# Kernel optimization log

Hardware: AMD Instinct MI355X
Metric: run time of the kernel (lower is better)

The kernel has to match this reference:

```python
import jax, jax.numpy as jnp
import numpy as np
import math


def _extend(chunk):
    # chunk: [b, C, w, 1, dh] -> stacked (prev, cur, next) chunks: [b, C, w, 1, dh, 3]
    prev = jnp.pad(chunk[:, :-1], ((0, 0), (1, 0), (0, 0), (0, 0), (0, 0)))
    nxt = jnp.pad(chunk[:, 1:], ((0, 0), (0, 1), (0, 0), (0, 0), (0, 0)))
    return jnp.stack((prev, chunk, nxt), axis=-1)


def local_xl_attention(q, kv, Wq, Wkv, Wc, w):
    b, L, dm = q.shape
    dh = Wkv.shape[1] // 2          # d_head (w_kv projects to 2*d_head)
    nh = dm // dh                   # n_head
    C = L // w                      # number of chunks

    qp = (q @ Wq).reshape(b, L, nh, dh) / math.sqrt(dh)   # [b,L,nh,dh]
    kvp = kv @ Wkv                                         # [b,L,2*dh]
    k = kvp[..., :dh][:, :, None, :]                       # [b,L,1,dh] single KV head
    v = kvp[..., dh:][:, :, None, :]

    # sliding_chunks_matmul_qk (faithful to original einsum, incl. sum over z)
    cq = qp.reshape(b, C, w, nh, dh)
    ck_e = _extend(k.reshape(b, C, w, 1, dh))              # [b,C,w,1,dh,3]
    attn = jnp.einsum('bcxhd,bzyode->bcxhey', cq, ck_e)    # [b,C,w,nh,3,w]
    attn = attn.reshape(b, L, nh, 3 * w)

    probs = jax.nn.softmax(attn, axis=-1)

    # sliding_chunks_matmul_pv (faithful, incl. sum over z)
    cp = probs.reshape(b, C, w, nh, 3, w)
    cv_e = _extend(v.reshape(b, C, w, 1, dh))              # [b,C,w,1,dh,3]
    ctx = jnp.einsum('bcwhpd,bzdoep->bcwhe', cp, cv_e)     # [b,C,w,nh,dh]
    out = ctx.reshape(b, L, dm) @ Wc
    return out


def setup_inputs() -> dict:
    key = jax.random.key(0)
    ks = jax.random.split(key, 5)
    B, L, DM, NH = 1, 4096, 1024, 16
    DH = DM // NH
    scale = 0.02
    return {
        'q': jax.random.normal(ks[0], (B, L, DM), dtype=jnp.float32),
        'kv': jax.random.normal(ks[1], (B, L, DM), dtype=jnp.float32),
        'Wq': jax.random.normal(ks[2], (DM, DM), dtype=jnp.float32) * scale,
        'Wkv': jax.random.normal(ks[3], (DM, 2 * DH), dtype=jnp.float32) * scale,
        'Wc': jax.random.normal(ks[4], (DM, DM), dtype=jnp.float32) * scale,
        'w': 512,
    }


def reference(q, kv, Wq, Wkv, Wc, w):
    return local_xl_attention(q, kv, Wq, Wkv, Wc, w)
```

## Files before the change

kernel.cpp:

```cpp
#include <hip/hip_runtime.h>
#include <hip/hip_bf16.h>
#include <cstdint>
#include <cstddef>

#define L_ 4096
#define DM_ 1024
#define NH_ 16
#define DH_ 64
#define W_ 512
#define C_ 8
#define W3_ 1536
#define NROWS_ 65536

typedef __attribute__((ext_vector_type(8))) short short8;
typedef __attribute__((ext_vector_type(4))) float f32x4;

__device__ __forceinline__ void async16(const void* g, void* l) {
    __builtin_amdgcn_global_load_lds(
        (const __attribute__((address_space(1))) unsigned int*)g,
        (__attribute__((address_space(3))) unsigned int*)l, 16, 0, 0);
}

#if __has_builtin(__builtin_amdgcn_exp2f)
#define FEXP2(x) __builtin_amdgcn_exp2f(x)
#else
#define FEXP2(x) exp2f(x)
#endif

__device__ __forceinline__ int nanhit(unsigned u) {
    return (((u & 0x7F80u) == 0x7F80u) | (((u >> 16) & 0x7F80u) == 0x7F80u));
}
__global__ __launch_bounds__(256) void detect_kernel(const uint4* __restrict__ q,
                                                     int* __restrict__ flag) {
    __shared__ int s;
    if (threadIdx.x == 0) s = 0;
    __syncthreads();
    int hit = 0;
#pragma unroll
    for (int r = 0; r < 8; ++r) {
        uint4 v = q[threadIdx.x + 256 * r];
        hit |= nanhit(v.x) | nanhit(v.y) | nanhit(v.z) | nanhit(v.w);
    }
    if (__any(hit)) { if ((threadIdx.x & 63) == 0) atomicOr(&s, 1); }
    __syncthreads();
    if (threadIdx.x == 0) flag[0] = s;
}

__device__ __forceinline__ float ldf(const void* X, size_t i, int f32) {
    return f32 ? ((const float*)X)[i] : __bfloat162float(((const __hip_bfloat16*)X)[i]);
}

__global__ __launch_bounds__(256) void megaprep(const void* __restrict__ q,
                                                const void* __restrict__ kv,
                                                const void* __restrict__ Wq,
                                                const void* __restrict__ Wkv,
                                                const void* __restrict__ Wc,
                                                __hip_bfloat16* __restrict__ qbuf,
                                                __hip_bfloat16* __restrict__ WqT,
                                                __hip_bfloat16* __restrict__ WkvT,
                                                __hip_bfloat16* __restrict__ WcT,
                                                __hip_bfloat16* __restrict__ kvred,
                                                const int* __restrict__ flag) {
    __shared__ float t[64][65];
    const int b = blockIdx.x;
    const int f32 = flag[0];
    const int tid = threadIdx.x;

    if (b < 4096) {
        int i = (b * 256 + tid) * 4;
        if (f32) {
            float4 v = *(const float4*)((const float*)q + i);
            __hip_bfloat162 tmp[2] = {__float22bfloat162_rn({v.x, v.y}),
                                      __float22bfloat162_rn({v.z, v.w})};
            *(short4*)((short*)qbuf + i) = *(const short4*)tmp;
        } else {
            *(short4*)((short*)qbuf + i) = *(const short4*)((const short*)q + i);
        }
    } else if (b < 4640) {
        const void* W;
        __hip_bfloat16* WT;
        int K = 1024, N, n0, k0;
        if (b < 4352) {
            int bx = b - 4096; W = Wq; WT = WqT; N = 1024;
            n0 = (bx & 15) * 64; k0 = (bx >> 4) * 64;
        } else if (b < 4608) {
            int bx = b - 4352; W = Wc; WT = WcT; N = 1024;
            n0 = (bx & 15) * 64; k0 = (bx >> 4) * 64;
        } else {
            int bx = b - 4608; W = Wkv; WT = WkvT; N = 128;
            n0 = (bx & 1) * 64; k0 = (bx >> 1) * 64;
        }
        const int tx = tid & 63;
        const int ty = tid >> 6;
#pragma unroll
        for (int r = 0; r < 16; ++r) {
            int k = ty + r * 4;
            t[k][tx] = ldf(W, (size_t)(k0 + k) * N + n0 + tx, f32);
        }
        __syncthreads();
#pragma unroll
        for (int r = 0; r < 16; ++r) {
            int n = ty + r * 4;
            WT[(size_t)(n0 + n) * K + k0 + tx] = __float2bfloat16(t[tx][n]);
        }
    } else {
        int y2 = b - 4640;
        int c = tid * 4;
        float a0 = 0.f, a1 = 0.f, a2 = 0.f, a3 = 0.f;
        if (y2 < 512) {
#pragma unroll
            for (int z = 0; z < C_; ++z) {
                size_t base = (size_t)(z * W_ + y2) * 1024 + c;
                a0 += ldf(kv, base + 0, f32);
                a1 += ldf(kv, base + 1, f32);
                a2 += ldf(kv, base + 2, f32);
                a3 += ldf(kv, base + 3, f32);
            }
        } else {
            int row = (y2 < 1024) ? (y2 - 512) : (3584 + y2 - 1024);
            size_t base = (size_t)row * 1024 + c;
            a0 = ldf(kv, base + 0, f32);
            a1 = ldf(kv, base + 1, f32);
            a2 = ldf(kv, base + 2, f32);
            a3 = ldf(kv, base + 3, f32);
        }
        __hip_bfloat162 tmp[2] = {__float22bfloat162_rn({a0, a1}),
                                  __float22bfloat162_rn({a2, a3})};
        *(short4*)((short*)kvred + (size_t)y2 * 1024 + c) = *(const short4*)tmp;
    }
}

struct GemmP {
    const __hip_bfloat16* A;
    const __hip_bfloat16* BT;
    void* C;
    int M, N, K;
    float alpha;
    int cMode;
    int ntiles;
    int swz;
    int nblocks;
};

__global__ __launch_bounds__(256) void gemm_bt_mfma(GemmP p0, GemmP p1,
                                                    const int* __restrict__ flag) {
    __shared__ __hip_bfloat16 Asl[2][128 * 32];
    __shared__ __hip_bfloat16 Bsl[2][64 * 32];

    GemmP p;
    int bid;
    if ((int)blockIdx.x < p0.nblocks) { p = p0; bid = blockIdx.x; }
    else { p = p1; bid = (int)blockIdx.x - p0.nblocks; }

    int mt, nt;
    if (!p.swz) { mt = bid / p.ntiles; nt = bid % p.ntiles; }
    else {
        int g = bid / (8 * p.ntiles);
        int rem = bid % (8 * p.ntiles);
        mt = g * 8 + (rem & 7);
        nt = rem >> 3;
    }
    const int m0 = mt * 128;
    const int n0 = nt * 64;
    const int K = p.K;
    const int N = p.N;

    const int tid = threadIdx.x;
    const int lane = tid & 63;
    const int wv = tid >> 6;
    const int wm = wv >> 1;
    const int wn = wv & 1;
    const int col = lane & 15;
    const int quad = lane >> 4;

    const int srow = lane >> 2;
    const int scol = (lane & 3) * 8;
    const __hip_bfloat16* Ag = p.A + (size_t)m0 * K;
    const __hip_bfloat16* Bg = p.BT + (size_t)n0 * K;

    f32x4 acc[4][2] = {};

    for (int k0 = 0; k0 < K; k0 += 64) {
#pragma unroll
        for (int h = 0; h < 2; ++h) {
            int arow = wv * 32 + h * 16 + srow;
#pragma unroll
            for (int kc = 0; kc < 2; ++kc)
                async16(Ag + (size_t)arow * K + k0 + kc * 32 + scol,
                        &Asl[kc][arow * 32 + scol]);
        }
        {
            int brow = wv * 16 + srow;
#pragma unroll
            for (int kc = 0; kc < 2; ++kc)
                async16(Bg + (size_t)brow * K + k0 + kc * 32 + scol,
                        &Bsl[kc][brow * 32 + scol]);
        }
        __syncthreads();

#pragma unroll
        for (int kc = 0; kc < 2; ++kc) {
            short8 af[4], bfr[2];
#pragma unroll
            for (int i = 0; i < 4; ++i)
                af[i] = *(const short8*)(&Asl[kc][(wm * 64 + i * 16 + col) * 32 + quad * 8]);
#pragma unroll
            for (int j = 0; j < 2; ++j)
                bfr[j] = *(const short8*)(&Bsl[kc][(wn * 32 + j * 16 + col) * 32 + quad * 8]);
#pragma unroll
            for (int am = 0; am < 4; ++am)
#pragma unroll
                for (int bn = 0; bn < 2; ++bn)
                    acc[am][bn] = __builtin_amdgcn_mfma_f32_16x16x32_bf16(af[am], bfr[bn], acc[am][bn], 0, 0, 0);
        }
        __syncthreads();
    }

    int cF = (p.cMode == 1) ? 1 : ((p.cMode == 2) ? 0 : flag[0]);
#pragma unroll
    for (int am = 0; am < 4; ++am)
#pragma unroll
        for (int bn = 0; bn < 2; ++bn)
#pragma unroll
            for (int r = 0; r < 4; ++r) {
                size_t ci = (size_t)(m0 + wm * 64 + am * 16 + quad * 4 + r) * N
                            + n0 + wn * 32 + bn * 16 + col;
                float v = acc[am][bn][r] * p.alpha;
                if (cF) ((float*)p.C)[ci] = v;
                else ((__hip_bfloat16*)p.C)[ci] = __float2bfloat16(v);
            }
}

__global__ __launch_bounds__(256) void sums_kernel(const float* __restrict__ kvp_red,
                                                   __hip_bfloat16* __restrict__ Kb,
                                                   __hip_bfloat16* __restrict__ Vt) {
    int t = blockIdx.x * 256 + threadIdx.x;
    int d = t & 63;
    int y = t >> 6;

    float kc = kvp_red[(size_t)y * 128 + d];
    float kf = kvp_red[(size_t)(512 + y) * 128 + d];
    float kl = kvp_red[(size_t)(1024 + y) * 128 + d];
    float vc = kvp_red[(size_t)y * 128 + 64 + d];
    float vf = kvp_red[(size_t)(512 + y) * 128 + 64 + d];
    float vl = kvp_red[(size_t)(1024 + y) * 128 + 64 + d];

    float kvals[3] = {kc - kl, kc, kc - kf};
    float vvals[3] = {vc - vl, vc, vc - vf};
#pragma unroll
    for (int e = 0; e < 3; ++e) {
        int key = e * W_ + y;
        Kb[(size_t)key * 64 + d] = __float2bfloat16(kvals[e]);
        int g = key >> 6;
        int i = key & 63;
        int p = ((i & 15) << 2) | (i >> 4);
        Vt[(size_t)d * W3_ + g * 64 + p] = __float2bfloat16(vvals[e]);
    }
}

#define PSTRIDE 72
__global__ __launch_bounds__(256, 2) void attn_kernel(const __hip_bfloat16* __restrict__ qb,
                                                      const __hip_bfloat16* __restrict__ Kb,
                                                      const __hip_bfloat16* __restrict__ Vt,
                                                      __hip_bfloat16* __restrict__ ctx) {
    __shared__ __align__(16) char smem[36864 + 1024];
    float* Ls = (float*)smem;
    float* lsum = (float*)(smem + 36864);

    const int tid = threadIdx.x;
    const int lane = tid & 63;
    const int wv = tid >> 6;
    const int m0 = blockIdx.x * 64;
    const int col = lane & 15;
    const int quad = lane >> 4;
    __hip_bfloat16* pw = (__hip_bfloat16*)smem + wv * (64 * PSTRIDE);

    short8 qf[4][2];
#pragma unroll
    for (int rg = 0; rg < 4; ++rg) {
        const __hip_bfloat16* qp = qb + (size_t)(m0 + rg * 16 + col) * 64 + quad * 8;
        qf[rg][0] = *(const short8*)(qp);
        qf[rg][1] = *(const short8*)(qp + 32);
    }

    f32x4 O[4][4] = {};
    float lrow[4][4] = {};

    for (int t = 0; t < 6; ++t) {
        const int kt = wv * 384 + t * 64;

        short8 kb0[4], kb1[4];
#pragma unroll
        for (int f = 0; f < 4; ++f) {
            const __hip_bfloat16* kp = Kb + (size_t)(kt + f * 16 + col) * 64 + quad * 8;
            kb0[f] = *(const short8*)(kp);
            kb1[f] = *(const short8*)(kp + 32);
        }

#pragma unroll
        for (int rg = 0; rg < 4; ++rg) {
            f32x4 S[4];
            __builtin_amdgcn_s_setprio(1);
#pragma unroll
            for (int f = 0; f < 4; ++f) {
                f32x4 s = {};
                s = __builtin_amdgcn_mfma_f32_16x16x32_bf16(qf[rg][0], kb0[f], s, 0, 0, 0);
                s = __builtin_amdgcn_mfma_f32_16x16x32_bf16(qf[rg][1], kb1[f], s, 0, 0, 0);
                S[f] = s;
            }
            __builtin_amdgcn_s_setprio(0);
#pragma unroll
            for (int f = 0; f < 4; ++f)
#pragma unroll
                for (int r = 0; r < 4; ++r) S[f][r] = FEXP2(S[f][r]);
#pragma unroll
            for (int r = 0; r < 4; ++r)
                lrow[rg][r] += (S[0][r] + S[1][r]) + (S[2][r] + S[3][r]);
#pragma unroll
            for (int r = 0; r < 4; ++r) {
                __hip_bfloat162 p01 = __float22bfloat162_rn({S[0][r], S[1][r]});
                __hip_bfloat162 p23 = __float22bfloat162_rn({S[2][r], S[3][r]});
                short4 t4;
                *(__hip_bfloat162*)(&t4.x) = p01;
                *(__hip_bfloat162*)(&t4.z) = p23;
                *(short4*)(pw + (rg * 16 + quad * 4 + r) * PSTRIDE + col * 4) = t4;
            }
        }

        short8 vb0[4], vb1[4];
#pragma unroll
        for (int f = 0; f < 4; ++f) {
            const __hip_bfloat16* vp = Vt + (size_t)(f * 16 + col) * W3_ + kt + quad * 8;
            vb0[f] = *(const short8*)(vp);
            vb1[f] = *(const short8*)(vp + 32);
        }

#pragma unroll
        for (int rg = 0; rg < 4; ++rg) {
            short8 a0 = *(const short8*)(pw + (rg * 16 + col) * PSTRIDE + quad * 8);
            short8 a1 = *(const short8*)(pw + (rg * 16 + col) * PSTRIDE + 32 + quad * 8);
            __builtin_amdgcn_s_setprio(1);
#pragma unroll
            for (int f = 0; f < 4; ++f) {
                O[rg][f] = __builtin_amdgcn_mfma_f32_16x16x32_bf16(a0, vb0[f], O[rg][f], 0, 0, 0);
                O[rg][f] = __builtin_amdgcn_mfma_f32_16x16x32_bf16(a1, vb1[f], O[rg][f], 0, 0, 0);
            }
            __builtin_amdgcn_s_setprio(0);
        }
    }

#pragma unroll
    for (int msk = 1; msk <= 8; msk <<= 1)
#pragma unroll
        for (int rg = 0; rg < 4; ++rg)
#pragma unroll
            for (int r = 0; r < 4; ++r) lrow[rg][r] += __shfl_xor(lrow[rg][r], msk, 64);

    __syncthreads();

    if (col == 0) {
#pragma unroll
        for (int rg = 0; rg < 4; ++rg)
#pragma unroll
            for (int r = 0; r < 4; ++r)
                lsum[wv * 64 + rg * 16 + quad * 4 + r] = lrow[rg][r];
    }

#pragma unroll
    for (int half = 0; half < 2; ++half) {
#pragma unroll
        for (int g = 0; g < 2; ++g) {
            int rg = half * 2 + g;
#pragma unroll
            for (int f = 0; f < 4; ++f)
#pragma unroll
                for (int r = 0; r < 4; ++r)
                    Ls[(wv * 32 + g * 16 + quad * 4 + r) * 66 + f * 16 + col] = O[rg][f][r];
        }
        __syncthreads();
#pragma unroll
        for (int i = 0; i < 8; ++i) {
            int r32 = wv * 8 + i;
            int row = half * 32 + r32;
            float tot = Ls[(0 * 32 + r32) * 66 + lane]
                      + Ls[(1 * 32 + r32) * 66 + lane]
                      + Ls[(2 * 32 + r32) * 66 + lane]
                      + Ls[(3 * 32 + r32) * 66 + lane];
            float ltot = lsum[0 * 64 + row] + lsum[1 * 64 + row]
                       + lsum[2 * 64 + row] + lsum[3 * 64 + row];
            ctx[(size_t)(m0 + row) * 64 + lane] = __float2bfloat16(tot * (1.f / ltot));
        }
        __syncthreads();
    }
}

extern "C" void kernel_launch(void* const* d_in, const int* in_sizes, int n_in,
                              void* d_out, int out_size, void* d_ws, size_t ws_size,
                              hipStream_t stream) {
    const void* q   = d_in[0];
    const void* kv  = d_in[1];
    const void* Wq  = d_in[2];
    const void* Wkv = d_in[3];
    const void* Wc  = d_in[4];

    char* ws = (char*)d_ws;
    size_t off = 0;
    int* flag = (int*)(ws + off); off += 1024;
    __hip_bfloat16* qbuf   = (__hip_bfloat16*)(ws + off); off += (size_t)L_ * DM_ * 2;
    __hip_bfloat16* WqT    = (__hip_bfloat16*)(ws + off); off += (size_t)DM_ * DM_ * 2;
    __hip_bfloat16* WkvT   = (__hip_bfloat16*)(ws + off); off += (size_t)128 * DM_ * 2;
    __hip_bfloat16* WcT    = (__hip_bfloat16*)(ws + off); off += (size_t)DM_ * DM_ * 2;
    __hip_bfloat16* qb     = (__hip_bfloat16*)(ws + off); off += (size_t)L_ * DM_ * 2;
    __hip_bfloat16* kvred  = (__hip_bfloat16*)(ws + off); off += (size_t)1536 * 1024 * 2;
    float*          kvpred = (float*)(ws + off);          off += (size_t)1536 * 128 * 4;
    __hip_bfloat16* Kb     = (__hip_bfloat16*)(ws + off); off += (size_t)W3_ * 64 * 2;
    __hip_bfloat16* Vt     = (__hip_bfloat16*)(ws + off); off += (size_t)64 * W3_ * 2;
    __hip_bfloat16* ctxb   = (__hip_bfloat16*)(ws + off);

    detect_kernel<<<1, 256, 0, stream>>>((const uint4*)q, flag);

    megaprep<<<6176, 256, 0, stream>>>(q, kv, Wq, Wkv, Wc,
                                       qbuf, WqT, WkvT, WcT, kvred, flag);

    {
        GemmP pq{qbuf, WqT, (void*)qb, L_, DM_, DM_,
                 0.125f * 1.44269504f, 2, 16, 1, 512};
        GemmP pk{kvred, WkvT, (void*)kvpred, 1536, 128, DM_,
                 1.0f, 1, 2, 0, 24};
        gemm_bt_mfma<<<536, 256, 0, stream>>>(pq, pk, flag);
    }
    sums_kernel<<<128, 256, 0, stream>>>(kvpred, Kb, Vt);
    attn_kernel<<<dim3(NROWS_ / 64), 256, 0, stream>>>(qb, Kb, Vt, ctxb);
    {
        GemmP pc{ctxb, WcT, d_out, L_, DM_, DM_, 1.0f, 0, 16, 1, 512};
        GemmP pnull{};
        pnull.nblocks = 0;
        gemm_bt_mfma<<<512, 256, 0, stream>>>(pc, pnull, flag);
    }
}
```

Before: 200.7 us.

## Split attention work by query rows per wave instead of key ranges

```diff
diff --git a/kernel.cpp b/kernel.cpp
--- a/kernel.cpp
+++ b/kernel.cpp
@@ -259,35 +259,32 @@
 }
 
 #define PSTRIDE 72
-__global__ __launch_bounds__(256, 2) void attn_kernel(const __hip_bfloat16* __restrict__ qb,
+__global__ __launch_bounds__(256, 4) void attn_kernel(const __hip_bfloat16* __restrict__ qb,
                                                       const __hip_bfloat16* __restrict__ Kb,
                                                       const __hip_bfloat16* __restrict__ Vt,
                                                       __hip_bfloat16* __restrict__ ctx) {
-    __shared__ __align__(16) char smem[36864 + 1024];
-    float* Ls = (float*)smem;
-    float* lsum = (float*)(smem + 36864);
+    __shared__ __align__(16) __hip_bfloat16 psm[4][16 * PSTRIDE];
 
     const int tid = threadIdx.x;
     const int lane = tid & 63;
     const int wv = tid >> 6;
-    const int m0 = blockIdx.x * 64;
+    const int m0 = blockIdx.x * 64 + wv * 16;
     const int col = lane & 15;
     const int quad = lane >> 4;
-    __hip_bfloat16* pw = (__hip_bfloat16*)smem + wv * (64 * PSTRIDE);
-
-    short8 qf[4][2];
-#pragma unroll
-    for (int rg = 0; rg < 4; ++rg) {
-        const __hip_bfloat16* qp = qb + (size_t)(m0 + rg * 16 + col) * 64 + quad * 8;
-        qf[rg][0] = *(const short8*)(qp);
-        qf[rg][1] = *(const short8*)(qp + 32);
-    }
-
-    f32x4 O[4][4] = {};
-    float lrow[4][4] = {};
-
-    for (int t = 0; t < 6; ++t) {
-        const int kt = wv * 384 + t * 64;
+    __hip_bfloat16* pw = psm[wv];
+
+    short8 qf0, qf1;
+    {
+        const __hip_bfloat16* qp = qb + (size_t)(m0 + col) * 64 + quad * 8;
+        qf0 = *(const short8*)(qp);
+        qf1 = *(const short8*)(qp + 32);
+    }
+
+    f32x4 O[4] = {};
+    float lrow[4] = {};
+
+    for (int t = 0; t < 24; ++t) {
+        const int kt = t * 64;
 
         short8 kb0[4], kb1[4];
 #pragma unroll
@@ -297,34 +294,31 @@
             kb1[f] = *(const short8*)(kp + 32);
         }
 
-#pragma unroll
-        for (int rg = 0; rg < 4; ++rg) {
-            f32x4 S[4];
-            __builtin_amdgcn_s_setprio(1);
-#pragma unroll
-            for (int f = 0; f < 4; ++f) {
-                f32x4 s = {};
-                s = __builtin_amdgcn_mfma_f32_16x16x32_bf16(qf[rg][0], kb0[f], s, 0, 0, 0);
-                s = __builtin_amdgcn_mfma_f32_16x16x32_bf16(qf[rg][1], kb1[f], s, 0, 0, 0);
-                S[f] = s;
-            }
-            __builtin_amdgcn_s_setprio(0);
-#pragma unroll
-            for (int f = 0; f < 4; ++f)
-#pragma unroll
-                for (int r = 0; r < 4; ++r) S[f][r] = FEXP2(S[f][r]);
-#pragma unroll
-            for (int r = 0; r < 4; ++r)
-                lrow[rg][r] += (S[0][r] + S[1][r]) + (S[2][r] + S[3][r]);
-#pragma unroll
-            for (int r = 0; r < 4; ++r) {
-                __hip_bfloat162 p01 = __float22bfloat162_rn({S[0][r], S[1][r]});
-                __hip_bfloat162 p23 = __float22bfloat162_rn({S[2][r], S[3][r]});
-                short4 t4;
-                *(__hip_bfloat162*)(&t4.x) = p01;
-                *(__hip_bfloat162*)(&t4.z) = p23;
-                *(short4*)(pw + (rg * 16 + quad * 4 + r) * PSTRIDE + col * 4) = t4;
-            }
+        f32x4 S[4];
+        __builtin_amdgcn_s_setprio(1);
+#pragma unroll
+        for (int f = 0; f < 4; ++f) {
+            f32x4 s = {};
+            s = __builtin_amdgcn_mfma_f32_16x16x32_bf16(qf0, kb0[f], s, 0, 0, 0);
+            s = __builtin_amdgcn_mfma_f32_16x16x32_bf16(qf1, kb1[f], s, 0, 0, 0);
+            S[f] = s;
+        }
+        __builtin_amdgcn_s_setprio(0);
+#pragma unroll
+        for (int f = 0; f < 4; ++f)
+#pragma unroll
+            for (int r = 0; r < 4; ++r) S[f][r] = FEXP2(S[f][r]);
+#pragma unroll
+        for (int r = 0; r < 4; ++r)
+            lrow[r] += (S[0][r] + S[1][r]) + (S[2][r] + S[3][r]);
+#pragma unroll
+        for (int r = 0; r < 4; ++r) {
+            __hip_bfloat162 p01 = __float22bfloat162_rn({S[0][r], S[1][r]});
+            __hip_bfloat162 p23 = __float22bfloat162_rn({S[2][r], S[3][r]});
+            short4 t4;
+            *(__hip_bfloat162*)(&t4.x) = p01;
+            *(__hip_bfloat162*)(&t4.z) = p23;
+            *(short4*)(pw + (quad * 4 + r) * PSTRIDE + col * 4) = t4;
         }
 
         short8 vb0[4], vb1[4];
@@ -335,62 +329,29 @@
             vb1[f] = *(const short8*)(vp + 32);
         }
 
-#pragma unroll
-        for (int rg = 0; rg < 4; ++rg) {
-            short8 a0 = *(const short8*)(pw + (rg * 16 + col) * PSTRIDE + quad * 8);
-            short8 a1 = *(const short8*)(pw + (rg * 16 + col) * PSTRIDE + 32 + quad * 8);
-            __builtin_amdgcn_s_setprio(1);
-#pragma unroll
-            for (int f = 0; f < 4; ++f) {
-                O[rg][f] = __builtin_amdgcn_mfma_f32_16x16x32_bf16(a0, vb0[f], O[rg][f], 0, 0, 0);
-                O[rg][f] = __builtin_amdgcn_mfma_f32_16x16x32_bf16(a1, vb1[f], O[rg][f], 0, 0, 0);
-            }
-            __builtin_amdgcn_s_setprio(0);
-        }
+        short8 a0 = *(const short8*)(pw + col * PSTRIDE + quad * 8);
+        short8 a1 = *(const short8*)(pw + col * PSTRIDE + 32 + quad * 8);
+        __builtin_amdgcn_s_setprio(1);
+#pragma unroll
+        for (int f = 0; f < 4; ++f) {
+            O[f] = __builtin_amdgcn_mfma_f32_16x16x32_bf16(a0, vb0[f], O[f], 0, 0, 0);
+            O[f] = __builtin_amdgcn_mfma_f32_16x16x32_bf16(a1, vb1[f], O[f], 0, 0, 0);
+        }
+        __builtin_amdgcn_s_setprio(0);
     }
 
 #pragma unroll
     for (int msk = 1; msk <= 8; msk <<= 1)
 #pragma unroll
-        for (int rg = 0; rg < 4; ++rg)
-#pragma unroll
-            for (int r = 0; r < 4; ++r) lrow[rg][r] += __shfl_xor(lrow[rg][r], msk, 64);
-
-    __syncthreads();
-
-    if (col == 0) {
-#pragma unroll
-        for (int rg = 0; rg < 4; ++rg)
-#pragma unroll
-            for (int r = 0; r < 4; ++r)
-                lsum[wv * 64 + rg * 16 + quad * 4 + r] = lrow[rg][r];
-    }
-
-#pragma unroll
-    for (int half = 0; half < 2; ++half) {
-#pragma unroll
-        for (int g = 0; g < 2; ++g) {
-            int rg = half * 2 + g;
-#pragma unroll
-            for (int f = 0; f < 4; ++f)
-#pragma unroll
-                for (int r = 0; r < 4; ++r)
-                    Ls[(wv * 32 + g * 16 + quad * 4 + r) * 66 + f * 16 + col] = O[rg][f][r];
-        }
-        __syncthreads();
-#pragma unroll
-        for (int i = 0; i < 8; ++i) {
-            int r32 = wv * 8 + i;
-            int row = half * 32 + r32;
-            float tot = Ls[(0 * 32 + r32) * 66 + lane]
-                      + Ls[(1 * 32 + r32) * 66 + lane]
-                      + Ls[(2 * 32 + r32) * 66 + lane]
-                      + Ls[(3 * 32 + r32) * 66 + lane];
-            float ltot = lsum[0 * 64 + row] + lsum[1 * 64 + row]
-                       + lsum[2 * 64 + row] + lsum[3 * 64 + row];
-            ctx[(size_t)(m0 + row) * 64 + lane] = __float2bfloat16(tot * (1.f / ltot));
-        }
-        __syncthreads();
+        for (int r = 0; r < 4; ++r) lrow[r] += __shfl_xor(lrow[r], msk, 64);
+
+#pragma unroll
+    for (int r = 0; r < 4; ++r) {
+        float inv = 1.f / lrow[r];
+#pragma unroll
+        for (int f = 0; f < 4; ++f)
+            ctx[(size_t)(m0 + quad * 4 + r) * 64 + f * 16 + col] =
+                __float2bfloat16(O[f][r] * inv);
     }
 }
 
```

After: 315.8 us. 1.57x slower.
